# Performance work log

Hardware: AMD Instinct MI355X
Metric: run time of the kernel (lower is better)

Reference implementation:

```python
import jax, jax.numpy as jnp
import numpy as np

B, T, D = 4, 4096, 1024

def setup_inputs() -> dict:
    key = jax.random.key(0)
    ks = jax.random.split(key, 8)
    s = 1.0 / np.sqrt(D)
    return {
        "x": jax.random.normal(ks[0], (B, T, D), dtype=jnp.float32),
        # diagonal SSM params (per-channel)
        "A": jax.random.uniform(ks[1], (D,), dtype=jnp.float32, minval=0.5, maxval=0.99),  # stable decay
        "Bp": jax.random.normal(ks[2], (D,), dtype=jnp.float32) * 0.1,
        "Cp": jax.random.normal(ks[3], (D,), dtype=jnp.float32),
        # gate Linear
        "gate_w": jax.random.uniform(ks[4], (D, D), dtype=jnp.float32, minval=-s, maxval=s),
        "gate_b": jnp.zeros((D,), dtype=jnp.float32),
        # out Linear
        "out_w": jax.random.uniform(ks[5], (D, D), dtype=jnp.float32, minval=-s, maxval=s),
        "out_b": jnp.zeros((D,), dtype=jnp.float32),
    }

def _ssm(x, A, Bp, Cp):
    # diagonal linear recurrence: h_t = A*h_{t-1} + Bp*x_t ; y_t = Cp*h_t
    bx = x * Bp  # (B,T,D)
    def step(h, bx_t):
        h = A * h + bx_t  # (B,D)
        return h, h
    h0 = jnp.zeros((x.shape[0], x.shape[2]), dtype=x.dtype)
    _, hs = jax.lax.scan(step, h0, jnp.swapaxes(bx, 0, 1))  # (T,B,D)
    return jnp.swapaxes(hs, 0, 1) * Cp  # (B,T,D)

def reference(x, A, Bp, Cp, gate_w, gate_b, out_w, out_b):
    ssm_out = _ssm(x, A, Bp, Cp)
    gate = jax.nn.sigmoid(jnp.einsum('btd,ed->bte', x, gate_w) + gate_b)
    y = gate * ssm_out
    return jnp.einsum('btd,ed->bte', y, out_w) + out_b
```

## Files before the change

### kernel.cpp

```cpp
#include <hip/hip_runtime.h>
#include <hip/hip_bf16.h>
#include <cstdio>

typedef __hip_bfloat16 bf16;
typedef __bf16 bf16x8 __attribute__((ext_vector_type(8)));
typedef float f32x4 __attribute__((ext_vector_type(4)));

#define B_DIM 4
#define T_DIM 4096
#define D_DIM 1024
#define NC 64
#define LC 64

#define M_DIM (B_DIM * T_DIM)
#define BM 256
#define BN 256
#define BK 32
#define NT (D_DIM / BK)
#define GM (M_DIM / BM)
#define GN (D_DIM / BN)

__global__ __launch_bounds__(256) void cast_w_kernel(
    const float* __restrict__ gw, const float* __restrict__ ow,
    bf16* __restrict__ gw16, bf16* __restrict__ ow16, int n) {
  int i = blockIdx.x * 256 + threadIdx.x;
  if (i < n) {
    gw16[i] = __float2bfloat16(gw[i]);
    ow16[i] = __float2bfloat16(ow[i]);
  }
}

__global__ __launch_bounds__(256) void ssm_pass1(
    const float* __restrict__ x, const float* __restrict__ A,
    const float* __restrict__ Bp, float* __restrict__ hfin) {
  const int tid  = threadIdx.x;
  const int dblk = blockIdx.x & 3;
  const int c    = (blockIdx.x >> 2) & (NC - 1);
  const int b    = blockIdx.x >> 8;
  const int d    = dblk * 256 + tid;
  const float a = A[d], bp = Bp[d];
  const float* p = x + ((size_t)(b * T_DIM + c * LC) * D_DIM + d);
  float h = 0.f;
#pragma unroll 4
  for (int i = 0; i < LC; ++i)
    h = fmaf(a, h, bp * p[(size_t)i * D_DIM]);
  hfin[(b * NC + c) * D_DIM + d] = h;
}

__global__ __launch_bounds__(256) void ssm_pass2(
    const float* __restrict__ A, const float* __restrict__ hfin,
    float* __restrict__ hin) {
  const int idx = blockIdx.x * 256 + threadIdx.x;
  const int d = idx & (D_DIM - 1);
  const int b = idx >> 10;
  float aL = A[d];
#pragma unroll
  for (int s = 0; s < 6; ++s) aL *= aL;
  float h = 0.f;
  for (int c = 0; c < NC; ++c) {
    const int o = (b * NC + c) * D_DIM + d;
    hin[o] = h;
    h = fmaf(aL, h, hfin[o]);
  }
}

__global__ __launch_bounds__(256) void ssm_pass3(
    const float* __restrict__ x, const float* __restrict__ A,
    const float* __restrict__ Bp, const float* __restrict__ Cp,
    const float* __restrict__ hin, bf16* __restrict__ ssm16,
    bf16* __restrict__ x16) {
  const int tid  = threadIdx.x;
  const int dblk = blockIdx.x & 3;
  const int c    = (blockIdx.x >> 2) & (NC - 1);
  const int b    = blockIdx.x >> 8;
  const int d    = dblk * 256 + tid;
  const float a = A[d], bp = Bp[d], cp = Cp[d];
  float h = hin[(b * NC + c) * D_DIM + d];
  const size_t base = (size_t)(b * T_DIM + c * LC) * D_DIM + d;
#pragma unroll 4
  for (int i = 0; i < LC; ++i) {
    const size_t o = base + (size_t)i * D_DIM;
    const float xv = x[o];
    h = fmaf(a, h, bp * xv);
    ssm16[o] = __float2bfloat16(cp * h);
    x16[o]  = __float2bfloat16(xv);
  }
}

template <bool GATE>
__global__ __launch_bounds__(512) void gemm256(
    const bf16* __restrict__ Xm, const bf16* __restrict__ Wm,
    const float* __restrict__ bias, const bf16* __restrict__ ssm,
    bf16* __restrict__ Ybf, float* __restrict__ Yf) {
  __shared__ __align__(16) short LDS[4][16384];

  const int tid  = threadIdx.x;
  const int lane = tid & 63;
  const int wave = tid >> 6;
  const int wm = wave >> 2;
  const int wn = wave & 3;
  const int l15 = lane & 15;
  const int sA = ((lane >> 4) ^ ((l15 >> 1) & 3)) << 3;

  const int bid = blockIdx.x;
  const int swz = (bid & 7) * (GM * GN / 8) + (bid >> 3);
  const int m0 = (swz >> 2) * BM;
  const int n0 = (swz & 3) * BN;

  const int row0 = tid >> 2;
  const int c0   = (tid & 3) ^ ((row0 >> 1) & 3);
  const size_t offA0 = (size_t)(m0 + row0) * D_DIM + c0 * 8;
  const size_t offB0 = (size_t)(n0 + row0) * D_DIM + c0 * 8;

  auto gll = [](const bf16* g, short* l) {
    __builtin_amdgcn_global_load_lds(
        (const __attribute__((address_space(1))) void*)g,
        (__attribute__((address_space(3))) void*)l, 16, 0, 0);
  };
  auto STAGE = [&](int buf, int kt) {
    const size_t ko = (size_t)kt * BK;
    short* b0 = &LDS[buf][0] + wave * 512;
    gll(Xm + offA0 + ko,               b0);
    gll(Xm + offA0 + 128 * D_DIM + ko, b0 + 4096);
    gll(Wm + offB0 + ko,               b0 + 8192);
    gll(Wm + offB0 + 128 * D_DIM + ko, b0 + 12288);
  };

  f32x4 acc[8][4] = {};

  STAGE(0, 0);
  STAGE(1, 1);
  STAGE(2, 2);

#define KTILE_BODY(T_, VM_N, DO_STAGE)                                      \
  {                                                                         \
    asm volatile("s_waitcnt vmcnt(" #VM_N ")" ::: "memory");                \
    __builtin_amdgcn_s_barrier();                                           \
    if (DO_STAGE) STAGE(((T_) + 3) & 3, (T_) + 3);                          \
    const short* bb = &LDS[(T_) & 3][0];                                    \
    bf16x8 a[8], b[4];                                                      \
    _Pragma("unroll")                                                       \
    for (int i = 0; i < 8; ++i)                                             \
      a[i] = *(const bf16x8*)(bb + (wm * 128 + i * 16 + l15) * BK + sA);    \
    _Pragma("unroll")                                                       \
    for (int j = 0; j < 4; ++j)                                             \
      b[j] = *(const bf16x8*)(bb + 8192 + (wn * 64 + j * 16 + l15) * BK + sA); \
    asm volatile("s_waitcnt lgkmcnt(0)" ::: "memory");                      \
    __builtin_amdgcn_sched_barrier(0);                                      \
    __builtin_amdgcn_s_setprio(1);                                          \
    _Pragma("unroll")                                                       \
    for (int i = 0; i < 8; ++i)                                             \
      _Pragma("unroll")                                                     \
      for (int j = 0; j < 4; ++j)                                           \
        acc[i][j] =                                                         \
            __builtin_amdgcn_mfma_f32_16x16x32_bf16(a[i], b[j], acc[i][j], 0, 0, 0); \
    __builtin_amdgcn_s_setprio(0);                                          \
    __builtin_amdgcn_s_barrier();                                           \
  }

  for (int t = 0; t < NT - 3; ++t)
    KTILE_BODY(t, 8, true);
  KTILE_BODY(NT - 3, 8, false);
  KTILE_BODY(NT - 2, 4, false);
  KTILE_BODY(NT - 1, 0, false);
#undef KTILE_BODY

#pragma unroll
  for (int i = 0; i < 8; ++i) {
#pragma unroll
    for (int j = 0; j < 4; ++j) {
      const int col = n0 + wn * 64 + j * 16 + l15;
      const float bv = bias[col];
#pragma unroll
      for (int v = 0; v < 4; ++v) {
        const int row = m0 + wm * 128 + i * 16 + (lane >> 4) * 4 + v;
        const size_t o = (size_t)row * D_DIM + col;
        const float val = acc[i][j][v] + bv;
        if (GATE) {
          const float g = 1.f / (1.f + expf(-val));
          Ybf[o] = __float2bfloat16(g * __bfloat162float(ssm[o]));
        } else {
          Yf[o] = val;
        }
      }
    }
  }
}

extern "C" void kernel_launch(void* const* d_in, const int* in_sizes, int n_in,
                              void* d_out, int out_size, void* d_ws, size_t ws_size,
                              hipStream_t stream) {
  const float* x  = (const float*)d_in[0];
  const float* A  = (const float*)d_in[1];
  const float* Bp = (const float*)d_in[2];
  const float* Cp = (const float*)d_in[3];
  const float* gw = (const float*)d_in[4];
  const float* gb = (const float*)d_in[5];
  const float* ow = (const float*)d_in[6];
  const float* ob = (const float*)d_in[7];
  float* out = (float*)d_out;

  const size_t NEED = 73400320;
  if (ws_size < NEED) {
    fprintf(stderr, "kernel_launch: ws_size %zu < needed %zu\n", ws_size, NEED);
    return;
  }
  char* ws = (char*)d_ws;
  bf16*  x16   = (bf16*)(ws);
  bf16*  ssm16 = (bf16*)(ws + 33554432);
  bf16*  gw16  = (bf16*)(ws + 67108864);
  bf16*  ow16  = (bf16*)(ws + 69206016);
  float* hfin  = (float*)(ws + 71303168);
  float* hin   = (float*)(ws + 72351744);

  cast_w_kernel<<<(D_DIM * D_DIM) / 256, 256, 0, stream>>>(gw, ow, gw16, ow16, D_DIM * D_DIM);
  ssm_pass1<<<B_DIM * NC * (D_DIM / 256), 256, 0, stream>>>(x, A, Bp, hfin);
  ssm_pass2<<<(B_DIM * D_DIM) / 256, 256, 0, stream>>>(A, hfin, hin);
  ssm_pass3<<<B_DIM * NC * (D_DIM / 256), 256, 0, stream>>>(x, A, Bp, Cp, hin, ssm16, x16);

  gemm256<true><<<GM * GN, 512, 0, stream>>>(x16, gw16, gb, ssm16, ssm16, nullptr);
  gemm256<false><<<GM * GN, 512, 0, stream>>>(ssm16, ow16, ob, nullptr, nullptr, out);
}
```

Before: 136.8 us.

## Restructure GEMM mainloop into 64-wide K steps with phased interleaved staging

```diff
diff --git a/kernel.cpp b/kernel.cpp
--- a/kernel.cpp
+++ b/kernel.cpp
@@ -15,8 +15,8 @@
 #define M_DIM (B_DIM * T_DIM)
 #define BM 256
 #define BN 256
-#define BK 32
-#define NT (D_DIM / BK)
+#define KSTEP 64
+#define NS (D_DIM / KSTEP)
 #define GM (M_DIM / BM)
 #define GN (D_DIM / BN)
 
@@ -92,7 +92,7 @@
     const bf16* __restrict__ Xm, const bf16* __restrict__ Wm,
     const float* __restrict__ bias, const bf16* __restrict__ ssm,
     bf16* __restrict__ Ybf, float* __restrict__ Yf) {
-  __shared__ __align__(16) short LDS[4][16384];
+  __shared__ __align__(16) short LDS[2][32768];
 
   const int tid  = threadIdx.x;
   const int lane = tid & 63;
@@ -100,70 +100,100 @@
   const int wm = wave >> 2;
   const int wn = wave & 3;
   const int l15 = lane & 15;
-  const int sA = ((lane >> 4) ^ ((l15 >> 1) & 3)) << 3;
+  const int lg  = lane >> 4;
+  const int l7  = lane & 7;
 
   const int bid = blockIdx.x;
   const int swz = (bid & 7) * (GM * GN / 8) + (bid >> 3);
   const int m0 = (swz >> 2) * BM;
   const int n0 = (swz & 3) * BN;
 
-  const int row0 = tid >> 2;
-  const int c0   = (tid & 3) ^ ((row0 >> 1) & 3);
-  const size_t offA0 = (size_t)(m0 + row0) * D_DIM + c0 * 8;
-  const size_t offB0 = (size_t)(n0 + row0) * D_DIM + c0 * 8;
-
-  auto gll = [](const bf16* g, short* l) {
+  const int rowOff  = tid >> 3;
+  const int slotOff = ((tid & 7) ^ ((tid >> 3) & 7)) * 8;
+
+  const int bCol0 = ((0 + lg) ^ l7) * 8;
+  const int bCol1 = ((4 + lg) ^ l7) * 8;
+  const int aRowBase = wm * 8192 + l15 * 64;
+  const int bRowBase = 16384 + (wn >> 1) * 8192 + ((wn & 1) * 64 + l15) * 64;
+
+  auto gll = [](const bf16* g, const short* l) {
     __builtin_amdgcn_global_load_lds(
         (const __attribute__((address_space(1))) void*)g,
         (__attribute__((address_space(3))) void*)l, 16, 0, 0);
   };
-  auto STAGE = [&](int buf, int kt) {
-    const size_t ko = (size_t)kt * BK;
-    short* b0 = &LDS[buf][0] + wave * 512;
-    gll(Xm + offA0 + ko,               b0);
-    gll(Xm + offA0 + 128 * D_DIM + ko, b0 + 4096);
-    gll(Wm + offB0 + ko,               b0 + 8192);
-    gll(Wm + offB0 + 128 * D_DIM + ko, b0 + 12288);
+  auto STAGE1 = [&](const bf16* P, int growbase, int ldsbase, int step) {
+    const size_t ko = (size_t)step * KSTEP;
+#pragma unroll
+    for (int g = 0; g < 2; ++g)
+      gll(P + (size_t)(growbase + 64 * g + rowOff) * D_DIM + ko + slotOff,
+          &LDS[0][0] + ldsbase + (g * 512 + wave * 64) * 8);
   };
 
   f32x4 acc[8][4] = {};
-
-  STAGE(0, 0);
-  STAGE(1, 1);
-  STAGE(2, 2);
-
-#define KTILE_BODY(T_, VM_N, DO_STAGE)                                      \
+  bf16x8 bfr[2][4];
+
+  STAGE1(Xm, m0,       0,             0);
+  STAGE1(Xm, m0 + 128, 8192,          0);
+  STAGE1(Wm, n0,       16384,         0);
+  STAGE1(Wm, n0 + 128, 24576,         0);
+  STAGE1(Wm, n0,       32768 + 16384, 1);
+  STAGE1(Wm, n0 + 128, 32768 + 24576, 1);
+  asm volatile("s_waitcnt vmcnt(4)" ::: "memory");
+  __builtin_amdgcn_s_barrier();
+
+#define MFMA_ __builtin_amdgcn_mfma_f32_16x16x32_bf16
+#define PHASE(RB_, P_, DO_STAGE_, SPTR_, SROW_, SLDS_, SSTEP_, DO_VM_, VM_, DO_BAR_) \
   {                                                                         \
-    asm volatile("s_waitcnt vmcnt(" #VM_N ")" ::: "memory");                \
+    const short* bb = &LDS[0][0] + (RB_) * 32768;                           \
+    if ((P_) == 0) {                                                        \
+      _Pragma("unroll")                                                     \
+      for (int j = 0; j < 4; ++j) {                                         \
+        bfr[0][j] = *(const bf16x8*)(bb + bRowBase + j * 1024 + bCol0);     \
+        bfr[1][j] = *(const bf16x8*)(bb + bRowBase + j * 1024 + bCol1);     \
+      }                                                                     \
+    }                                                                       \
+    bf16x8 a00 = *(const bf16x8*)(bb + aRowBase + (2*(P_)) * 1024 + bCol0); \
+    bf16x8 a01 = *(const bf16x8*)(bb + aRowBase + (2*(P_)) * 1024 + bCol1); \
+    bf16x8 a10 = *(const bf16x8*)(bb + aRowBase + (2*(P_)+1) * 1024 + bCol0); \
+    bf16x8 a11 = *(const bf16x8*)(bb + aRowBase + (2*(P_)+1) * 1024 + bCol1); \
+    if (DO_STAGE_) STAGE1(SPTR_, SROW_, SLDS_, SSTEP_);                     \
+    if (DO_VM_) asm volatile("s_waitcnt " VM_ ::: "memory");                \
     __builtin_amdgcn_s_barrier();                                           \
-    if (DO_STAGE) STAGE(((T_) + 3) & 3, (T_) + 3);                          \
-    const short* bb = &LDS[(T_) & 3][0];                                    \
-    bf16x8 a[8], b[4];                                                      \
-    _Pragma("unroll")                                                       \
-    for (int i = 0; i < 8; ++i)                                             \
-      a[i] = *(const bf16x8*)(bb + (wm * 128 + i * 16 + l15) * BK + sA);    \
-    _Pragma("unroll")                                                       \
-    for (int j = 0; j < 4; ++j)                                             \
-      b[j] = *(const bf16x8*)(bb + 8192 + (wn * 64 + j * 16 + l15) * BK + sA); \
     asm volatile("s_waitcnt lgkmcnt(0)" ::: "memory");                      \
     __builtin_amdgcn_sched_barrier(0);                                      \
     __builtin_amdgcn_s_setprio(1);                                          \
     _Pragma("unroll")                                                       \
-    for (int i = 0; i < 8; ++i)                                             \
-      _Pragma("unroll")                                                     \
-      for (int j = 0; j < 4; ++j)                                           \
-        acc[i][j] =                                                         \
-            __builtin_amdgcn_mfma_f32_16x16x32_bf16(a[i], b[j], acc[i][j], 0, 0, 0); \
+    for (int j = 0; j < 4; ++j) {                                           \
+      acc[2*(P_)][j]   = MFMA_(a00, bfr[0][j], acc[2*(P_)][j],   0, 0, 0);  \
+      acc[2*(P_)][j]   = MFMA_(a01, bfr[1][j], acc[2*(P_)][j],   0, 0, 0);  \
+      acc[2*(P_)+1][j] = MFMA_(a10, bfr[0][j], acc[2*(P_)+1][j], 0, 0, 0);  \
+      acc[2*(P_)+1][j] = MFMA_(a11, bfr[1][j], acc[2*(P_)+1][j], 0, 0, 0);  \
+    }                                                                       \
     __builtin_amdgcn_s_setprio(0);                                          \
-    __builtin_amdgcn_s_barrier();                                           \
-  }
-
-  for (int t = 0; t < NT - 3; ++t)
-    KTILE_BODY(t, 8, true);
-  KTILE_BODY(NT - 3, 8, false);
-  KTILE_BODY(NT - 2, 4, false);
-  KTILE_BODY(NT - 1, 0, false);
-#undef KTILE_BODY
+    if (DO_BAR_) __builtin_amdgcn_s_barrier();                              \
+  }
+
+  for (int i = 0; i < 7; ++i) {
+    const int s0 = 2 * i;
+    PHASE(0, 0, true, Xm, m0,       32768 + 0,     s0 + 1, false, "vmcnt(0)", true)
+    PHASE(0, 1, true, Xm, m0 + 128, 32768 + 8192,  s0 + 1, false, "vmcnt(0)", true)
+    PHASE(0, 2, true, Wm, n0,       16384,         s0 + 2, false, "vmcnt(0)", true)
+    PHASE(0, 3, true, Wm, n0 + 128, 24576,         s0 + 2, true,  "vmcnt(4)", true)
+    PHASE(1, 0, true, Xm, m0,       0,             s0 + 2, false, "vmcnt(0)", true)
+    PHASE(1, 1, true, Xm, m0 + 128, 8192,          s0 + 2, false, "vmcnt(0)", true)
+    PHASE(1, 2, true, Wm, n0,       32768 + 16384, s0 + 3, false, "vmcnt(0)", true)
+    PHASE(1, 3, true, Wm, n0 + 128, 32768 + 24576, s0 + 3, true,  "vmcnt(4)", true)
+  }
+  PHASE(0, 0, true,  Xm, m0,       32768 + 0,    15, false, "vmcnt(0)", true)
+  PHASE(0, 1, true,  Xm, m0 + 128, 32768 + 8192, 15, false, "vmcnt(0)", true)
+  PHASE(0, 2, false, Xm, 0, 0, 0,                    false, "vmcnt(0)", true)
+  PHASE(0, 3, false, Xm, 0, 0, 0,                    true,  "vmcnt(0)", true)
+  PHASE(1, 0, false, Xm, 0, 0, 0,                    false, "vmcnt(0)", true)
+  PHASE(1, 1, false, Xm, 0, 0, 0,                    false, "vmcnt(0)", true)
+  PHASE(1, 2, false, Xm, 0, 0, 0,                    false, "vmcnt(0)", true)
+  PHASE(1, 3, false, Xm, 0, 0, 0,                    false, "vmcnt(0)", false)
+#undef PHASE
+#undef MFMA_
 
 #pragma unroll
   for (int i = 0; i < 8; ++i) {
```

Result: faster. 129.2 us (-5.5%).
